# Kernel optimization log

Hardware: AMD Instinct MI355X
Metric: run time of the kernel (lower is better)

The kernel has to match this reference:

```python
import jax, jax.numpy as jnp
import numpy as np

# ---- config derived from init_kwargs (level=3, max_levels=14, max_size=256,
# max_channels=512, margin=10, start_cutoff=2, critical_layers=2, window_size=6) ----
SCALE_FACTOR = 2          # size_prev(16) < size(32)
UP_FACTOR = 2 * SCALE_FACTOR   # 4
UP_PAD = (13, 10)         # p = 24 - 2*sf = 20 -> ((p+1)//2 + 2*sf - 1, p//2)
DOWN_PAD = (5, 5)         # p = 12 - 2 = 10 -> ((p+1)//2, p//2)
MARGIN = 10
CUTOFF, BAND_HALF = 5.656854249492381, 10.343145750507619   # level 3, sr=128
CUTOFF_PREV, BAND_HALF_PREV = 4.0, 4.0                      # level 2, sr=128
SR = 32 * SCALE_FACTOR * 2  # 128


def _lowpass_filter(n_taps, cutoff, band_half, sr):
    # Kaiser-windowed sinc lowpass, identical math to the torch module.
    df = 2 * band_half / (sr / 2)
    atten = 2.285 * (n_taps - 1) * np.pi * df + 7.95
    if atten > 50:
        beta = 0.1102 * (atten - 8.7)
    elif atten >= 21:
        beta = 0.5842 * (atten - 21) ** 0.4 + 0.07886 * (atten - 21)
    else:
        beta = 0.0
    ind = np.arange(n_taps) - (n_taps - 1) / 2
    window = np.i0(beta * np.sqrt(1 - (2 * ind / (n_taps - 1)) ** 2)) / np.i0(beta)
    return 2 * cutoff / sr * np.sinc(2 * cutoff / sr * ind) * window


def setup_inputs() -> dict:
    key = jax.random.key(0)
    x = jax.random.normal(key, (16, 512, 36, 36), dtype=jnp.float32)
    up = _lowpass_filter(24, CUTOFF_PREV, BAND_HALF_PREV, SR)
    up = up / up.sum() * 2 * SCALE_FACTOR
    down = _lowpass_filter(12, CUTOFF, BAND_HALF, SR)
    down = down / down.sum()
    return {
        "x": x,
        "up_filter": jnp.asarray(up, dtype=jnp.float32),
        "down_filter": jnp.asarray(down, dtype=jnp.float32),
    }


def _upfirdn1d(x, kernel, up, down, pad, axis):
    # Separable 1D upfirdn along axis (2=H, 3=W) of NCHW tensor.
    # Matches upfirdn2d_native: zero-insert upsample (up-1 trailing zeros),
    # pad, correlate with flipped kernel, stride-`down` decimate.
    # lhs_dilation inserts up-1 zeros BETWEEN samples; adding up-1 to the
    # right pad reproduces the trailing zeros of the native op exactly.
    B, C, H, W = x.shape
    k = kernel.shape[0]
    w = jnp.flip(kernel).astype(x.dtype)
    if axis == 3:
        rhs = w.reshape(1, 1, 1, k)
        lhs_dil, strides = (1, up), (1, down)
        padding = ((0, 0), (pad[0], pad[1] + up - 1))
    else:
        rhs = w.reshape(1, 1, k, 1)
        lhs_dil, strides = (up, 1), (down, 1)
        padding = ((pad[0], pad[1] + up - 1), (0, 0))
    y = jax.lax.conv_general_dilated(
        x.reshape(B * C, 1, H, W), rhs,
        window_strides=strides, padding=padding, lhs_dilation=lhs_dil,
        dimension_numbers=("NCHW", "OIHW", "NCHW"))
    return y.reshape(B, C, y.shape[2], y.shape[3])


def reference(x, up_filter, down_filter):
    # Upsample x4 (separable: width then height)
    x = _upfirdn1d(x, up_filter, UP_FACTOR, 1, UP_PAD, axis=3)
    x = _upfirdn1d(x, up_filter, UP_FACTOR, 1, UP_PAD, axis=2)   # (16,512,144,144)
    # Pointwise nonlinearity in the high-res domain (alias-free)
    x = jax.nn.leaky_relu(x, 0.2)
    # Downsample x2 (separable: width then height)
    x = _upfirdn1d(x, down_filter, 1, 2, DOWN_PAD, axis=3)
    x = _upfirdn1d(x, down_filter, 1, 2, DOWN_PAD, axis=2)       # (16,512,72,72)
    m = SCALE_FACTOR * MARGIN // 2  # 10
    return x[:, :, m:-m, m:-m]      # (16,512,52,52)
```

## Files before the change

kernel.cpp:

```cpp
#include <hip/hip_runtime.h>


typedef float v2f __attribute__((ext_vector_type(2)));

static __device__ __forceinline__ v2f vsplat(float s) { v2f v; v.x = s; v.y = s; return v; }
#define VFMA(A, S, C) __builtin_elementwise_fma((A), vsplat(S), (C))

#define SCATTER(J, hv)                                                        \
    _Pragma("unroll")                                                         \
    for (int k = (J) & 1; k <= 11; k += 2) {                                  \
        if ((J) - k >= 0 && (((J) - k) >> 1) < 14)                            \
            acc[((J) - k) >> 1] = VFMA(hv, dn[11 - k], acc[((J) - k) >> 1]);  \
    }

#define DO_J(J, A, B, C, D, E, F)                                             \
    do {                                                                      \
        const int q_ = ((J) + 1) & 3;                                         \
        v2f h_ = (A) * vsplat(up[20 + q_]);                                   \
        h_ = VFMA((B), up[16 + q_], h_);                                      \
        h_ = VFMA((C), up[12 + q_], h_);                                      \
        h_ = VFMA((D), up[8 + q_], h_);                                       \
        h_ = VFMA((E), up[4 + q_], h_);                                       \
        h_ = VFMA((F), up[q_], h_);                                           \
        h_ = __builtin_elementwise_max(h_, h_ * vsplat(0.2f));                \
        SCATTER(J, h_);                                                       \
    } while (0)

#define GROUP(G, T0, T1, T2, T3, T4, T5)                                      \
    do {                                                                      \
        T0 = wbase[(G) + 5];                                                  \
        DO_J(4 * (G) - 1, T1, T2, T3, T4, T5, T0);                            \
        DO_J(4 * (G), T1, T2, T3, T4, T5, T0);                                \
        DO_J(4 * (G) + 1, T1, T2, T3, T4, T5, T0);                            \
        DO_J(4 * (G) + 2, T1, T2, T3, T4, T5, T0);                            \
    } while (0)

#define GROUP_TAIL(T0, T1, T2, T3, T4, T5)                                    \
    do {                                                                      \
        T0 = wbase[14];                                                       \
        DO_J(35, T1, T2, T3, T4, T5, T0);                                     \
        DO_J(36, T1, T2, T3, T4, T5, T0);                                     \
        DO_J(37, T1, T2, T3, T4, T5, T0);                                     \
    } while (0)

#define P3LD(RA, RB, M)                                                       \
    RA = p3b[(M)*53];                                                         \
    RB = p3b[((M) + 1) * 53];

#define P3OUT(J, A, B, C, D, E, F, G, H, I, JJ, K, L)                         \
    do {                                                                      \
        v2f a_ = (A) * vsplat(dn[11]);                                        \
        a_ = VFMA((B), dn[10], a_);                                           \
        a_ = VFMA((C), dn[9], a_);                                            \
        a_ = VFMA((D), dn[8], a_);                                            \
        a_ = VFMA((E), dn[7], a_);                                            \
        a_ = VFMA((F), dn[6], a_);                                            \
        a_ = VFMA((G), dn[5], a_);                                            \
        a_ = VFMA((H), dn[4], a_);                                            \
        a_ = VFMA((I), dn[3], a_);                                            \
        a_ = VFMA((JJ), dn[2], a_);                                           \
        a_ = VFMA((K), dn[1], a_);                                            \
        a_ = VFMA((L), dn[0], a_);                                            \
        const int oh_ = 7 * s + (J);                                          \
        if (oh_ < 52) {                                                       \
            op0[oh_ * 52 + ow] = a_.x;                                        \
            op1[oh_ * 52 + ow] = a_.y;                                        \
        }                                                                     \
    } while (0)

__global__ __launch_bounds__(512, 6)
void afa_kernel(const float* __restrict__ x,
                const float* __restrict__ upf,
                const float* __restrict__ dnf,
                float* __restrict__ out)
{
    __shared__ v2f buf[122 * 53];

    const int tid = threadIdx.x;
    const size_t q0 = (size_t)blockIdx.x * 2;
    const float* __restrict__ xp0 = x + q0 * 1296;
    const float* __restrict__ xp1 = xp0 + 1296;
    float* __restrict__ op0 = out + q0 * 2704;
    float* __restrict__ op1 = op0 + 2704;

    float up[24];
#pragma unroll
    for (int i = 0; i < 24; ++i) up[i] = upf[i];
    float dn[12];
#pragma unroll
    for (int i = 0; i < 12; ++i) dn[i] = dnf[i];

    if (tid < 510) {
        const int s1 = tid / 34;
        const int mw = tid % 34 + 1;

        v2f xr[8];
#pragma unroll
        for (int i = 0; i < 8; ++i) {
            int row = 2 * s1 + 1 + i;
            row = row > 35 ? 35 : row;
            xr[i].x = xp0[row * 36 + mw];
            xr[i].y = xp1[row * 36 + mw];
        }
#pragma unroll
        for (int j = 0; j < 8; ++j) {
            const int rel = ((j + 5) >> 2) - 1;
            const int c0  = 20 + ((j + 1) & 3);
            v2f a = vsplat(0.f);
#pragma unroll
            for (int t = 0; t < 6; ++t)
                a = VFMA(xr[rel + t], up[c0 - 4 * t], a);
            const int lh = 8 * s1 + j;
            if (lh < 114)
                buf[lh * 35 + (mw - 1)] = a;
        }
    }
    __syncthreads();

    const int  lh   = tid % 114;
    const int  p    = tid / 114;
    const bool act2 = tid < 456;
    v2f acc[14];
    if (act2) {
        const int L0 = 26 * p - ((p & 1) << 1);
        const v2f* __restrict__ wbase = &buf[lh * 35 + (L0 >> 2)];
        v2f w0 = wbase[0], w1 = wbase[1], w2 = wbase[2],
            w3 = wbase[3], w4 = wbase[4], w5 = wbase[5];
#pragma unroll
        for (int o = 0; o < 14; ++o) acc[o] = vsplat(0.f);

        DO_J(0, w0, w1, w2, w3, w4, w5);
        DO_J(1, w0, w1, w2, w3, w4, w5);
        DO_J(2, w0, w1, w2, w3, w4, w5);
        GROUP(1, w0, w1, w2, w3, w4, w5);
        GROUP(2, w1, w2, w3, w4, w5, w0);
        GROUP(3, w2, w3, w4, w5, w0, w1);
        GROUP(4, w3, w4, w5, w0, w1, w2);
        GROUP(5, w4, w5, w0, w1, w2, w3);
        GROUP(6, w5, w0, w1, w2, w3, w4);
        GROUP(7, w0, w1, w2, w3, w4, w5);
        GROUP(8, w1, w2, w3, w4, w5, w0);
        GROUP_TAIL(w2, w3, w4, w5, w0, w1);
    }
    __syncthreads();

    if (act2) {
        v2f* __restrict__ tw = &buf[lh * 53 + 13 * p];
        if (p & 1) {
#pragma unroll
            for (int oo = 0; oo < 13; ++oo) tw[oo] = acc[oo + 1];
        } else {
#pragma unroll
            for (int oo = 0; oo < 13; ++oo) tw[oo] = acc[oo];
        }
    }
    __syncthreads();

    if (tid < 416) {
        const int ow = tid % 52;
        const int s  = tid / 52;
        const v2f* __restrict__ p3b = &buf[(14 * s) * 53 + ow];

        v2f r0, r1, r2, r3, r4, r5, r6, r7, r8, r9, r10, r11;
        P3LD(r0, r1, 0)  P3LD(r2, r3, 2)  P3LD(r4, r5, 4)
        P3LD(r6, r7, 6)  P3LD(r8, r9, 8)  P3LD(r10, r11, 10)

        P3OUT(0, r0, r1, r2, r3, r4, r5, r6, r7, r8, r9, r10, r11);
        P3LD(r0, r1, 12)
        P3OUT(1, r2, r3, r4, r5, r6, r7, r8, r9, r10, r11, r0, r1);
        P3LD(r2, r3, 14)
        P3OUT(2, r4, r5, r6, r7, r8, r9, r10, r11, r0, r1, r2, r3);
        P3LD(r4, r5, 16)
        P3OUT(3, r6, r7, r8, r9, r10, r11, r0, r1, r2, r3, r4, r5);
        P3LD(r6, r7, 18)
        P3OUT(4, r8, r9, r10, r11, r0, r1, r2, r3, r4, r5, r6, r7);
        P3LD(r8, r9, 20)
        P3OUT(5, r10, r11, r0, r1, r2, r3, r4, r5, r6, r7, r8, r9);
        P3LD(r10, r11, 22)
        P3OUT(6, r0, r1, r2, r3, r4, r5, r6, r7, r8, r9, r10, r11);
    }
}

extern "C" void kernel_launch(void* const* d_in, const int* in_sizes, int n_in,
                              void* d_out, int out_size, void* d_ws, size_t ws_size,
                              hipStream_t stream)
{
    const float* x  = (const float*)d_in[0];
    const float* up = (const float*)d_in[1];
    const float* dn = (const float*)d_in[2];
    float* out = (float*)d_out;

    const int pairs = 16 * 512 / 2;
    afa_kernel<<<dim3(pairs), dim3(512), 0, stream>>>(x, up, dn, out);
}
```

Measured before the change: 154.4 us.

## Split each channel pair into two half-height blocks of 256 threads

Each block now handles half of the output rows (26 of 52) for a channel pair, so there are twice as many blocks of 256 threads, each using a smaller shared buffer. The goal is better occupancy and finer scheduling granularity, with less thread idling, compared with large 512-thread blocks. The trade-off is redundant halo work: each half recomputes overlapping upsampled rows, and the input rows are loaded twice. Register rotation in the vertical pass and in the final pass is also reworked.

Result: faster. 149.9 us (-2.9%).

```diff
diff --git a/kernel.cpp b/kernel.cpp
--- a/kernel.cpp
+++ b/kernel.cpp
@@ -2,82 +2,75 @@
 
 
 typedef float v2f __attribute__((ext_vector_type(2)));
-
-static __device__ __forceinline__ v2f vsplat(float s) { v2f v; v.x = s; v.y = s; return v; }
-#define VFMA(A, S, C) __builtin_elementwise_fma((A), vsplat(S), (C))
+static __device__ __forceinline__ v2f vsplat(float s){ v2f v; v.x=s; v.y=s; return v; }
+#define FMA2(A,S,C) __builtin_elementwise_fma((A), vsplat(S), (C))
 
 #define SCATTER(J, hv)                                                        \
     _Pragma("unroll")                                                         \
     for (int k = (J) & 1; k <= 11; k += 2) {                                  \
         if ((J) - k >= 0 && (((J) - k) >> 1) < 14)                            \
-            acc[((J) - k) >> 1] = VFMA(hv, dn[11 - k], acc[((J) - k) >> 1]);  \
+            acc2[((J) - k) >> 1] = FMA2(hv, dn[11 - k], acc2[((J) - k) >> 1]);\
     }
 
 #define DO_J(J, A, B, C, D, E, F)                                             \
     do {                                                                      \
         const int q_ = ((J) + 1) & 3;                                         \
         v2f h_ = (A) * vsplat(up[20 + q_]);                                   \
-        h_ = VFMA((B), up[16 + q_], h_);                                      \
-        h_ = VFMA((C), up[12 + q_], h_);                                      \
-        h_ = VFMA((D), up[8 + q_], h_);                                       \
-        h_ = VFMA((E), up[4 + q_], h_);                                       \
-        h_ = VFMA((F), up[q_], h_);                                           \
+        h_ = FMA2((B), up[16 + q_], h_);                                      \
+        h_ = FMA2((C), up[12 + q_], h_);                                      \
+        h_ = FMA2((D), up[8 + q_], h_);                                       \
+        h_ = FMA2((E), up[4 + q_], h_);                                       \
+        h_ = FMA2((F), up[q_], h_);                                           \
         h_ = __builtin_elementwise_max(h_, h_ * vsplat(0.2f));                \
         SCATTER(J, h_);                                                       \
     } while (0)
 
-#define GROUP(G, T0, T1, T2, T3, T4, T5)                                      \
+#define GROUPE(G, L, A, B, C, D, E, F)                                        \
     do {                                                                      \
-        T0 = wbase[(G) + 5];                                                  \
-        DO_J(4 * (G) - 1, T1, T2, T3, T4, T5, T0);                            \
-        DO_J(4 * (G), T1, T2, T3, T4, T5, T0);                                \
-        DO_J(4 * (G) + 1, T1, T2, T3, T4, T5, T0);                            \
-        DO_J(4 * (G) + 2, T1, T2, T3, T4, T5, T0);                            \
-    } while (0)
-
-#define GROUP_TAIL(T0, T1, T2, T3, T4, T5)                                    \
-    do {                                                                      \
-        T0 = wbase[14];                                                       \
-        DO_J(35, T1, T2, T3, T4, T5, T0);                                     \
-        DO_J(36, T1, T2, T3, T4, T5, T0);                                     \
-        DO_J(37, T1, T2, T3, T4, T5, T0);                                     \
+        L = wbase[(G) + 6];                                                   \
+        DO_J(4 * (G) - 1, A, B, C, D, E, F);                                  \
+        DO_J(4 * (G),     A, B, C, D, E, F);                                  \
+        DO_J(4 * (G) + 1, A, B, C, D, E, F);                                  \
+        DO_J(4 * (G) + 2, A, B, C, D, E, F);                                  \
     } while (0)
 
 #define P3LD(RA, RB, M)                                                       \
-    RA = p3b[(M)*53];                                                         \
-    RB = p3b[((M) + 1) * 53];
+    RA = t2b[(M) * 53];                                                       \
+    RB = t2b[((M) + 1) * 53];
 
 #define P3OUT(J, A, B, C, D, E, F, G, H, I, JJ, K, L)                         \
     do {                                                                      \
-        v2f a_ = (A) * vsplat(dn[11]);                                        \
-        a_ = VFMA((B), dn[10], a_);                                           \
-        a_ = VFMA((C), dn[9], a_);                                            \
-        a_ = VFMA((D), dn[8], a_);                                            \
-        a_ = VFMA((E), dn[7], a_);                                            \
-        a_ = VFMA((F), dn[6], a_);                                            \
-        a_ = VFMA((G), dn[5], a_);                                            \
-        a_ = VFMA((H), dn[4], a_);                                            \
-        a_ = VFMA((I), dn[3], a_);                                            \
-        a_ = VFMA((JJ), dn[2], a_);                                           \
-        a_ = VFMA((K), dn[1], a_);                                            \
-        a_ = VFMA((L), dn[0], a_);                                            \
-        const int oh_ = 7 * s + (J);                                          \
-        if (oh_ < 52) {                                                       \
+        if (7 * s3 + (J) < 26) {                                              \
+            v2f a_ = (A) * vsplat(dn[11]);                                    \
+            a_ = FMA2((B), dn[10], a_);                                       \
+            a_ = FMA2((C), dn[9], a_);                                        \
+            a_ = FMA2((D), dn[8], a_);                                        \
+            a_ = FMA2((E), dn[7], a_);                                        \
+            a_ = FMA2((F), dn[6], a_);                                        \
+            a_ = FMA2((G), dn[5], a_);                                        \
+            a_ = FMA2((H), dn[4], a_);                                        \
+            a_ = FMA2((I), dn[3], a_);                                        \
+            a_ = FMA2((JJ), dn[2], a_);                                       \
+            a_ = FMA2((K), dn[1], a_);                                        \
+            a_ = FMA2((L), dn[0], a_);                                        \
+            const int oh_ = 26 * hh + 7 * s3 + (J);                           \
             op0[oh_ * 52 + ow] = a_.x;                                        \
             op1[oh_ * 52 + ow] = a_.y;                                        \
         }                                                                     \
     } while (0)
 
-__global__ __launch_bounds__(512, 6)
+__global__ __launch_bounds__(256, 4)
 void afa_kernel(const float* __restrict__ x,
                 const float* __restrict__ upf,
                 const float* __restrict__ dnf,
                 float* __restrict__ out)
 {
-    __shared__ v2f buf[122 * 53];
+    __shared__ v2f buf[66 * 53];
 
     const int tid = threadIdx.x;
-    const size_t q0 = (size_t)blockIdx.x * 2;
+    const int bid = blockIdx.x;
+    const int hh  = bid & 1;
+    const size_t q0 = (size_t)(bid >> 1) * 2;
     const float* __restrict__ xp0 = x + q0 * 1296;
     const float* __restrict__ xp1 = xp0 + 1296;
     float* __restrict__ op0 = out + q0 * 2704;
@@ -90,94 +83,99 @@
 #pragma unroll
     for (int i = 0; i < 12; ++i) dn[i] = dnf[i];
 
-    if (tid < 510) {
+    if (tid < 204) {
         const int s1 = tid / 34;
         const int mw = tid % 34 + 1;
+        const int xb = 13 * hh + 3 * s1 + 1;
 
-        v2f xr[8];
+        v2f xr[9];
 #pragma unroll
-        for (int i = 0; i < 8; ++i) {
-            int row = 2 * s1 + 1 + i;
+        for (int i = 0; i < 9; ++i) {
+            int row = xb + i;
             row = row > 35 ? 35 : row;
             xr[i].x = xp0[row * 36 + mw];
             xr[i].y = xp1[row * 36 + mw];
         }
 #pragma unroll
-        for (int j = 0; j < 8; ++j) {
-            const int rel = ((j + 5) >> 2) - 1;
-            const int c0  = 20 + ((j + 1) & 3);
-            v2f a = vsplat(0.f);
+        for (int j = 0; j < 12; ++j) {
+            const int lh = 12 * s1 + j;
+            if (lh < 63) {
+                const int rel = ((j + 5) >> 2) - 1;
+                const int c0  = 20 + ((j + 1) & 3);
+                v2f a = vsplat(0.f);
 #pragma unroll
-            for (int t = 0; t < 6; ++t)
-                a = VFMA(xr[rel + t], up[c0 - 4 * t], a);
-            const int lh = 8 * s1 + j;
-            if (lh < 114)
+                for (int t = 0; t < 6; ++t)
+                    a = FMA2(xr[rel + t], up[c0 - 4 * t], a);
                 buf[lh * 35 + (mw - 1)] = a;
+            }
         }
     }
     __syncthreads();
 
-    const int  lh   = tid % 114;
-    const int  p    = tid / 114;
-    const bool act2 = tid < 456;
-    v2f acc[14];
+    const int  lh2  = tid % 63;
+    const int  p4   = tid / 63;
+    const bool act2 = tid < 252;
+    v2f acc2[14];
     if (act2) {
-        const int L0 = 26 * p - ((p & 1) << 1);
-        const v2f* __restrict__ wbase = &buf[lh * 35 + (L0 >> 2)];
+        const int L0 = 26 * p4 - ((p4 & 1) << 1);
+        const v2f* __restrict__ wbase = &buf[lh2 * 35 + (L0 >> 2)];
         v2f w0 = wbase[0], w1 = wbase[1], w2 = wbase[2],
-            w3 = wbase[3], w4 = wbase[4], w5 = wbase[5];
+            w3 = wbase[3], w4 = wbase[4], w5 = wbase[5], w6;
 #pragma unroll
-        for (int o = 0; o < 14; ++o) acc[o] = vsplat(0.f);
+        for (int o = 0; o < 14; ++o) acc2[o] = vsplat(0.f);
 
+        w6 = wbase[6];
         DO_J(0, w0, w1, w2, w3, w4, w5);
         DO_J(1, w0, w1, w2, w3, w4, w5);
         DO_J(2, w0, w1, w2, w3, w4, w5);
-        GROUP(1, w0, w1, w2, w3, w4, w5);
-        GROUP(2, w1, w2, w3, w4, w5, w0);
-        GROUP(3, w2, w3, w4, w5, w0, w1);
-        GROUP(4, w3, w4, w5, w0, w1, w2);
-        GROUP(5, w4, w5, w0, w1, w2, w3);
-        GROUP(6, w5, w0, w1, w2, w3, w4);
-        GROUP(7, w0, w1, w2, w3, w4, w5);
-        GROUP(8, w1, w2, w3, w4, w5, w0);
-        GROUP_TAIL(w2, w3, w4, w5, w0, w1);
+        GROUPE(1, w0, w1, w2, w3, w4, w5, w6);
+        GROUPE(2, w1, w2, w3, w4, w5, w6, w0);
+        GROUPE(3, w2, w3, w4, w5, w6, w0, w1);
+        GROUPE(4, w3, w4, w5, w6, w0, w1, w2);
+        GROUPE(5, w4, w5, w6, w0, w1, w2, w3);
+        GROUPE(6, w5, w6, w0, w1, w2, w3, w4);
+        GROUPE(7, w6, w0, w1, w2, w3, w4, w5);
+        GROUPE(8, w0, w1, w2, w3, w4, w5, w6);
+        DO_J(35, w2, w3, w4, w5, w6, w0);
+        DO_J(36, w2, w3, w4, w5, w6, w0);
+        DO_J(37, w2, w3, w4, w5, w6, w0);
     }
     __syncthreads();
 
     if (act2) {
-        v2f* __restrict__ tw = &buf[lh * 53 + 13 * p];
-        if (p & 1) {
+        v2f* __restrict__ tw = &buf[lh2 * 53 + 13 * p4];
+        if (p4 & 1) {
 #pragma unroll
-            for (int oo = 0; oo < 13; ++oo) tw[oo] = acc[oo + 1];
+            for (int oo = 0; oo < 13; ++oo) tw[oo] = acc2[oo + 1];
         } else {
 #pragma unroll
-            for (int oo = 0; oo < 13; ++oo) tw[oo] = acc[oo];
+            for (int oo = 0; oo < 13; ++oo) tw[oo] = acc2[oo];
         }
     }
     __syncthreads();
 
-    if (tid < 416) {
+    if (tid < 208) {
         const int ow = tid % 52;
-        const int s  = tid / 52;
-        const v2f* __restrict__ p3b = &buf[(14 * s) * 53 + ow];
+        const int s3 = tid / 52;
+        const v2f* __restrict__ t2b = &buf[(14 * s3) * 53 + ow];
 
-        v2f r0, r1, r2, r3, r4, r5, r6, r7, r8, r9, r10, r11;
-        P3LD(r0, r1, 0)  P3LD(r2, r3, 2)  P3LD(r4, r5, 4)
-        P3LD(r6, r7, 6)  P3LD(r8, r9, 8)  P3LD(r10, r11, 10)
+        v2f r0, r1, r2, r3, r4, r5, r6, r7, r8, r9, r10, r11, r12, r13, r14, r15;
+        P3LD(r0, r1, 0)   P3LD(r2, r3, 2)   P3LD(r4, r5, 4)
+        P3LD(r6, r7, 6)   P3LD(r8, r9, 8)   P3LD(r10, r11, 10)
+        P3LD(r12, r13, 12)
 
+        P3LD(r14, r15, 14)
         P3OUT(0, r0, r1, r2, r3, r4, r5, r6, r7, r8, r9, r10, r11);
-        P3LD(r0, r1, 12)
-        P3OUT(1, r2, r3, r4, r5, r6, r7, r8, r9, r10, r11, r0, r1);
-        P3LD(r2, r3, 14)
-        P3OUT(2, r4, r5, r6, r7, r8, r9, r10, r11, r0, r1, r2, r3);
-        P3LD(r4, r5, 16)
-        P3OUT(3, r6, r7, r8, r9, r10, r11, r0, r1, r2, r3, r4, r5);
-        P3LD(r6, r7, 18)
-        P3OUT(4, r8, r9, r10, r11, r0, r1, r2, r3, r4, r5, r6, r7);
-        P3LD(r8, r9, 20)
-        P3OUT(5, r10, r11, r0, r1, r2, r3, r4, r5, r6, r7, r8, r9);
-        P3LD(r10, r11, 22)
-        P3OUT(6, r0, r1, r2, r3, r4, r5, r6, r7, r8, r9, r10, r11);
+        P3LD(r0, r1, 16)
+        P3OUT(1, r2, r3, r4, r5, r6, r7, r8, r9, r10, r11, r12, r13);
+        P3LD(r2, r3, 18)
+        P3OUT(2, r4, r5, r6, r7, r8, r9, r10, r11, r12, r13, r14, r15);
+        P3LD(r4, r5, 20)
+        P3OUT(3, r6, r7, r8, r9, r10, r11, r12, r13, r14, r15, r0, r1);
+        P3LD(r6, r7, 22)
+        P3OUT(4, r8, r9, r10, r11, r12, r13, r14, r15, r0, r1, r2, r3);
+        P3OUT(5, r10, r11, r12, r13, r14, r15, r0, r1, r2, r3, r4, r5);
+        P3OUT(6, r12, r13, r14, r15, r0, r1, r2, r3, r4, r5, r6, r7);
     }
 }
 
@@ -190,6 +188,5 @@
     const float* dn = (const float*)d_in[2];
     float* out = (float*)d_out;
 
-    const int pairs = 16 * 512 / 2;
-    afa_kernel<<<dim3(pairs), dim3(512), 0, stream>>>(x, up, dn, out);
+    afa_kernel<<<dim3(16 * 512 / 2 * 2), dim3(256), 0, stream>>>(x, up, dn, out);
 }
```
